# Kernel tuning notes

Measured on AMD Instinct MI355X. Metric: run time of the kernel, lower is better.

## Reference

```python
import jax, jax.numpy as jnp
import numpy as np

D_MODEL = 768
D_INNER = 1536      # expand*d_model
D_STATE = 128
NHEADS = 12         # d_inner // headdim
HEADDIM = 128
D_CONV = 4
CONV_DIM = D_INNER + 2 * D_STATE   # 1792 (ngroups=1)
D_IN_PROJ = 2 * D_INNER + 2 * D_STATE + NHEADS  # 3340


def setup_inputs() -> dict:
    key = jax.random.key(0)
    it = iter(jax.random.split(key, 24))
    def rn(shape, s):
        return jax.random.normal(next(it), shape, jnp.float32) * s
    inp = {}
    inp['x'] = jax.random.normal(next(it), (8, 12, 4096), jnp.float32)
    # conv stem
    inp['w1'] = rn((192, 12, 5), 0.2); inp['b1'] = jnp.zeros((192,))
    inp['bn1_g'] = jnp.ones((192,)); inp['bn1_b'] = jnp.zeros((192,)); inp['bn1_m'] = jnp.zeros((192,)); inp['bn1_v'] = jnp.ones((192,))
    inp['w2'] = rn((384, 192, 3), 0.05); inp['b2'] = jnp.zeros((384,))
    inp['bn2_g'] = jnp.ones((384,)); inp['bn2_b'] = jnp.zeros((384,)); inp['bn2_m'] = jnp.zeros((384,)); inp['bn2_v'] = jnp.ones((384,))
    inp['w3'] = rn((768, 384, 3), 0.05); inp['b3'] = jnp.zeros((768,))
    inp['bn3_g'] = jnp.ones((768,)); inp['bn3_b'] = jnp.zeros((768,)); inp['bn3_m'] = jnp.zeros((768,)); inp['bn3_v'] = jnp.ones((768,))
    # Mamba2 backbone
    inp['in_proj_w'] = rn((D_IN_PROJ, D_MODEL), 0.02)
    inp['conv_w'] = rn((CONV_DIM, D_CONV), 0.2)
    inp['conv_b'] = jnp.zeros((CONV_DIM,))
    inp['dt_bias'] = rn((NHEADS,), 0.5)
    inp['A_log'] = jnp.log(jax.random.uniform(next(it), (NHEADS,), minval=1.0, maxval=16.0))
    inp['D'] = jnp.ones((NHEADS,))
    inp['norm_w'] = jnp.ones((D_INNER,))
    inp['out_proj_w'] = rn((D_MODEL, D_INNER), 0.02)
    # classifier
    inp['fc1_w'] = rn((1024, 768), 0.02); inp['fc1_b'] = jnp.zeros((1024,))
    inp['bnc_g'] = jnp.ones((1024,)); inp['bnc_b'] = jnp.zeros((1024,)); inp['bnc_m'] = jnp.zeros((1024,)); inp['bnc_v'] = jnp.ones((1024,))
    inp['fc2_w'] = rn((27, 1024), 0.02); inp['fc2_b'] = jnp.zeros((27,))
    return inp


def _conv1d(x, w, b, stride, pad):
    y = jax.lax.conv_general_dilated(x, w, (stride,), [(pad, pad)], dimension_numbers=('NCH', 'OIH', 'NCH'))
    return y + b[None, :, None]


def _bn(x, g, b, m, v, eps=1e-5):
    sh = (1, -1, 1) if x.ndim == 3 else (1, -1)
    return (x - m.reshape(sh)) * jax.lax.rsqrt(v.reshape(sh) + eps) * g.reshape(sh) + b.reshape(sh)


def _forward(x, w1, b1, bn1_g, bn1_b, bn1_m, bn1_v, w2, b2, bn2_g, bn2_b, bn2_m, bn2_v,
             w3, b3, bn3_g, bn3_b, bn3_m, bn3_v, in_proj_w, conv_w, conv_b, dt_bias,
             A_log, D, norm_w, out_proj_w, fc1_w, fc1_b, bnc_g, bnc_b, bnc_m, bnc_v, fc2_w, fc2_b):
    gelu = lambda t: jax.nn.gelu(t, approximate=False)
    # conv stem (B, 12, 4096) -> (B, 768, 1024)
    h = _bn(gelu(_conv1d(x, w1, b1, 2, 2)), bn1_g, bn1_b, bn1_m, bn1_v)
    h = _bn(gelu(_conv1d(h, w2, b2, 2, 1)), bn2_g, bn2_b, bn2_m, bn2_v)
    h = _bn(gelu(_conv1d(h, w3, b3, 1, 1)), bn3_g, bn3_b, bn3_m, bn3_v)
    u = h.transpose(0, 2, 1)  # (B, L, 768)
    # Mamba2
    zxbcdt = u @ in_proj_w.T  # (B, L, 3340)
    z = zxbcdt[..., :D_INNER]
    xBC = zxbcdt[..., D_INNER:D_INNER + CONV_DIM]
    dt = jax.nn.softplus(zxbcdt[..., D_INNER + CONV_DIM:] + dt_bias)  # (B, L, H)
    # causal depthwise conv over time + silu
    xc = jax.lax.conv_general_dilated(xBC.transpose(0, 2, 1), conv_w[:, None, :], (1,), [(D_CONV - 1, 0)],
                                      dimension_numbers=('NCH', 'OIH', 'NCH'), feature_group_count=CONV_DIM)
    xBC = jax.nn.silu(xc + conv_b[None, :, None]).transpose(0, 2, 1)
    xs = xBC[..., :D_INNER]
    Bm = xBC[..., D_INNER:D_INNER + D_STATE]   # (B, L, N), ngroups=1
    Cm = xBC[..., D_INNER + D_STATE:]
    A = -jnp.exp(A_log)  # (H,)
    b_, l_ = xs.shape[0], xs.shape[1]
    xh = xs.reshape(b_, l_, NHEADS, HEADDIM)
    dA = jnp.exp(dt * A)  # (B, L, H)
    tm = lambda t: jnp.moveaxis(t, 1, 0)
    def step(state, inps):
        x_t, dA_t, dt_t, B_t, C_t = inps
        # state: (B, H, P, N)
        state = state * dA_t[..., None, None] + (dt_t[..., None] * x_t)[..., None] * B_t[:, None, None, :]
        y_t = jnp.einsum('bhpn,bn->bhp', state, C_t)
        return state, y_t
    state0 = jnp.zeros((b_, NHEADS, HEADDIM, D_STATE), xs.dtype)
    _, ys = jax.lax.scan(step, state0, (tm(xh), tm(dA), tm(dt), tm(Bm), tm(Cm)))
    y = jnp.moveaxis(ys, 0, 1) + D[None, None, :, None] * xh  # (B, L, H, P)
    y = y.reshape(b_, l_, D_INNER)
    # gated RMSNorm (norm_before_gate=False)
    y = y * jax.nn.silu(z)
    y = y * jax.lax.rsqrt(jnp.mean(y * y, axis=-1, keepdims=True) + 1e-5) * norm_w
    out = y @ out_proj_w.T  # (B, L, 768)
    rep = out.mean(axis=1)
    h1 = jax.nn.relu(_bn(rep @ fc1_w.T + fc1_b, bnc_g, bnc_b, bnc_m, bnc_v))
    return h1 @ fc2_w.T + fc2_b


def reference(x, w1, b1, bn1_g, bn1_b, bn1_m, bn1_v, w2, b2, bn2_g, bn2_b, bn2_m, bn2_v,
              w3, b3, bn3_g, bn3_b, bn3_m, bn3_v, in_proj_w, conv_w, conv_b, dt_bias,
              A_log, D, norm_w, out_proj_w, fc1_w, fc1_b, bnc_g, bnc_b, bnc_m, bnc_v, fc2_w, fc2_b):
    return _forward(x, w1, b1, bn1_g, bn1_b, bn1_m, bn1_v, w2, b2, bn2_g, bn2_b, bn2_m, bn2_v,
                    w3, b3, bn3_g, bn3_b, bn3_m, bn3_v, in_proj_w, conv_w, conv_b, dt_bias,
                    A_log, D, norm_w, out_proj_w, fc1_w, fc1_b, bnc_g, bnc_b, bnc_m, bnc_v, fc2_w, fc2_b)
```

## Files before the change

kernel.cpp:

```cpp
#include <hip/hip_runtime.h>
#include <math.h>

#define DEV __device__ __forceinline__

DEV float geluf(float x){ return 0.5f*x*(1.0f+erff(x*0.7071067811865476f)); }
DEV float siluf(float x){ return x/(1.0f+expf(-x)); }
DEV float softplusf(float x){ return fmaxf(x,0.0f)+log1pf(expf(-fabsf(x))); }
DEV unsigned short f2bf(float f){
  unsigned int u = __float_as_uint(f);
  unsigned int r = (u + 0x7fffu + ((u>>16)&1u)) >> 16;
  return (unsigned short)r;
}

typedef __attribute__((ext_vector_type(8))) short short8;
typedef __attribute__((ext_vector_type(4))) float f32x4;

__global__ void conv1_k(const float* __restrict__ x, const float* __restrict__ w,
                        const float* __restrict__ bias,
                        const float* __restrict__ g, const float* __restrict__ bb,
                        const float* __restrict__ m, const float* __restrict__ v,
                        float* __restrict__ out){
  int t  = blockIdx.x*256 + threadIdx.x;
  int og = blockIdx.y;
  int b  = blockIdx.z;
  const float* xb = x + (size_t)b*12*4096;
  float acc[8];
  #pragma unroll
  for(int oo=0;oo<8;++oo) acc[oo] = bias[og*8+oo];
  for(int i=0;i<12;++i){
    float xv[5];
    #pragma unroll
    for(int k=0;k<5;++k){
      int src = 2*t + k - 2;
      xv[k] = (src>=0 && src<4096) ? xb[i*4096+src] : 0.0f;
    }
    #pragma unroll
    for(int oo=0;oo<8;++oo){
      const float* wr = w + (size_t)(og*8+oo)*60 + i*5;
      #pragma unroll
      for(int k=0;k<5;++k) acc[oo] = fmaf(wr[k], xv[k], acc[oo]);
    }
  }
  #pragma unroll
  for(int oo=0;oo<8;++oo){
    int o = og*8+oo;
    float y = geluf(acc[oo]);
    float sc = g[o]*rsqrtf(v[o]+1e-5f);
    y = (y-m[o])*sc + bb[o];
    out[(size_t)b*192*2048 + (size_t)o*2048 + t] = y;
  }
}

__global__ void xpose1_k(const float* __restrict__ h1, unsigned short* __restrict__ T1){
  __shared__ float tile[32][33];
  int t0 = blockIdx.x*32, i0 = blockIdx.y*32, b = blockIdx.z;
  int c = threadIdx.x & 31, r4 = threadIdx.x >> 5;
  const float* src = h1 + (size_t)b*393216;
  #pragma unroll
  for(int i=0;i<4;++i){ int r = r4 + i*8; tile[r][c] = src[(size_t)(i0+r)*2048 + t0 + c]; }
  __syncthreads();
  unsigned short* dst = T1 + (size_t)b*2048*192;
  #pragma unroll
  for(int i=0;i<4;++i){ int r = r4 + i*8;
    dst[(size_t)(t0+r)*192 + i0 + c] = f2bf(tile[c][r]);
  }
}

__global__ void wr2_k(const float* __restrict__ w, unsigned short* __restrict__ wr){
  int gid = blockIdx.x*256 + threadIdx.x;
  if(gid < 221184){
    int o = gid / 576, rem = gid - o*576, k = rem / 192, i = rem - k*192;
    wr[gid] = f2bf(w[(size_t)o*576 + i*3 + k]);
  }
}
__global__ void wr3_k(const float* __restrict__ w, unsigned short* __restrict__ wr){
  int gid = blockIdx.x*256 + threadIdx.x;
  if(gid < 884736){
    int o = gid / 1152, rem = gid - o*1152, k = rem / 384, i = rem - k*384;
    wr[gid] = f2bf(w[(size_t)o*1152 + i*3 + k]);
  }
}

__global__ __launch_bounds__(256) void conv2_mfma(const unsigned short* __restrict__ A,
                                                  const unsigned short* __restrict__ W,
                                                  const float* __restrict__ bias,
                                                  const float* __restrict__ g, const float* __restrict__ bb,
                                                  const float* __restrict__ bm, const float* __restrict__ bv,
                                                  unsigned short* __restrict__ outb){
  __shared__ unsigned short As[4096], Bs[4096];
  const int tid = threadIdx.x;
  const int lane = tid & 63, wave = tid >> 6;
  const int wm = wave & 1, wn = wave >> 1;
  const int m0 = blockIdx.y*128, n0 = blockIdx.x*128;
  const int bidx = m0 >> 10, tloc = m0 & 1023;
  f32x4 acc[4][4];
  #pragma unroll
  for(int i=0;i<4;++i)
    #pragma unroll
    for(int j=0;j<4;++j) acc[i][j] = (f32x4){0.f,0.f,0.f,0.f};
  const int u0 = tid, u1 = tid + 256;
  const int r0 = u0>>2, kl0 = (u0&3) ^ ((r0>>1)&3);
  const int r1 = u1>>2, kl1 = (u1&3) ^ ((r1>>1)&3);
  const int kg = lane>>4, ml = lane&15;
  const short8 z8 = {0,0,0,0,0,0,0,0};
  for(int kb=0; kb<3; ++kb){
    int ta = 2*(tloc + r0) + kb - 1;
    int tb = 2*(tloc + r1) + kb - 1;
    bool va = (ta>=0) && (ta<2048);
    bool vb = (tb>=0) && (tb<2048);
    const unsigned short* pa = A + ((size_t)bidx*2048 + ta)*192;
    const unsigned short* pb = A + ((size_t)bidx*2048 + tb)*192;
    for(int c0=0; c0<192; c0+=32){
      int k0 = kb*192 + c0;
      short8 a0 = va ? *reinterpret_cast<const short8*>(pa + c0 + kl0*8) : z8;
      short8 a1 = vb ? *reinterpret_cast<const short8*>(pb + c0 + kl1*8) : z8;
      short8 b0 = *reinterpret_cast<const short8*>(W + (size_t)(n0+r0)*576 + k0 + kl0*8);
      short8 b1 = *reinterpret_cast<const short8*>(W + (size_t)(n0+r1)*576 + k0 + kl1*8);
      __syncthreads();
      *reinterpret_cast<short8*>(As + u0*8) = a0;
      *reinterpret_cast<short8*>(As + u1*8) = a1;
      *reinterpret_cast<short8*>(Bs + u0*8) = b0;
      *reinterpret_cast<short8*>(Bs + u1*8) = b1;
      __syncthreads();
      short8 af[4], bfr[4];
      #pragma unroll
      for(int f=0;f<4;++f){
        int row = wm*64 + f*16 + ml;
        int un  = row*4 + (kg ^ ((row>>1)&3));
        af[f] = *reinterpret_cast<const short8*>(As + un*8);
        int rowb = wn*64 + f*16 + ml;
        int ub   = rowb*4 + (kg ^ ((rowb>>1)&3));
        bfr[f] = *reinterpret_cast<const short8*>(Bs + ub*8);
      }
      #pragma unroll
      for(int i=0;i<4;++i)
        #pragma unroll
        for(int j=0;j<4;++j)
          acc[i][j] = __builtin_amdgcn_mfma_f32_16x16x32_bf16(af[i], bfr[j], acc[i][j], 0, 0, 0);
    }
  }
  #pragma unroll
  for(int i=0;i<4;++i){
    int rb = m0 + wm*64 + i*16 + kg*4;
    #pragma unroll
    for(int j=0;j<4;++j){
      int col = n0 + wn*64 + j*16 + ml;
      float sc = g[col]*rsqrtf(bv[col]+1e-5f);
      float mm = bm[col], bbv = bb[col], bi = bias[col];
      #pragma unroll
      for(int r=0;r<4;++r){
        float yv = geluf(acc[i][j][r] + bi);
        yv = (yv - mm)*sc + bbv;
        outb[(size_t)(rb+r)*384 + col] = f2bf(yv);
      }
    }
  }
}

__global__ __launch_bounds__(256) void conv3_mfma(const unsigned short* __restrict__ A,
                                                  const unsigned short* __restrict__ W,
                                                  const float* __restrict__ bias,
                                                  const float* __restrict__ g, const float* __restrict__ bb,
                                                  const float* __restrict__ bm, const float* __restrict__ bv,
                                                  unsigned short* __restrict__ outb,
                                                  float* __restrict__ outf){
  __shared__ unsigned short As[4096], Bs[4096];
  const int tid = threadIdx.x;
  const int lane = tid & 63, wave = tid >> 6;
  const int wm = wave & 1, wn = wave >> 1;
  const int m0 = blockIdx.y*128, n0 = blockIdx.x*128;
  const int bidx = m0 >> 10, tloc = m0 & 1023;
  f32x4 acc[4][4];
  #pragma unroll
  for(int i=0;i<4;++i)
    #pragma unroll
    for(int j=0;j<4;++j) acc[i][j] = (f32x4){0.f,0.f,0.f,0.f};
  const int u0 = tid, u1 = tid + 256;
  const int r0 = u0>>2, kl0 = (u0&3) ^ ((r0>>1)&3);
  const int r1 = u1>>2, kl1 = (u1&3) ^ ((r1>>1)&3);
  const int kg = lane>>4, ml = lane&15;
  const short8 z8 = {0,0,0,0,0,0,0,0};
  for(int kb=0; kb<3; ++kb){
    int ta = tloc + r0 + kb - 1;
    int tb = tloc + r1 + kb - 1;
    bool va = (ta>=0) && (ta<1024);
    bool vb = (tb>=0) && (tb<1024);
    const unsigned short* pa = A + ((size_t)bidx*1024 + ta)*384;
    const unsigned short* pb = A + ((size_t)bidx*1024 + tb)*384;
    for(int c0=0; c0<384; c0+=32){
      int k0 = kb*384 + c0;
      short8 a0 = va ? *reinterpret_cast<const short8*>(pa + c0 + kl0*8) : z8;
      short8 a1 = vb ? *reinterpret_cast<const short8*>(pb + c0 + kl1*8) : z8;
      short8 b0 = *reinterpret_cast<const short8*>(W + (size_t)(n0+r0)*1152 + k0 + kl0*8);
      short8 b1 = *reinterpret_cast<const short8*>(W + (size_t)(n0+r1)*1152 + k0 + kl1*8);
      __syncthreads();
      *reinterpret_cast<short8*>(As + u0*8) = a0;
      *reinterpret_cast<short8*>(As + u1*8) = a1;
      *reinterpret_cast<short8*>(Bs + u0*8) = b0;
      *reinterpret_cast<short8*>(Bs + u1*8) = b1;
      __syncthreads();
      short8 af[4], bfr[4];
      #pragma unroll
      for(int f=0;f<4;++f){
        int row = wm*64 + f*16 + ml;
        int un  = row*4 + (kg ^ ((row>>1)&3));
        af[f] = *reinterpret_cast<const short8*>(As + un*8);
        int rowb = wn*64 + f*16 + ml;
        int ub   = rowb*4 + (kg ^ ((rowb>>1)&3));
        bfr[f] = *reinterpret_cast<const short8*>(Bs + ub*8);
      }
      #pragma unroll
      for(int i=0;i<4;++i)
        #pragma unroll
        for(int j=0;j<4;++j)
          acc[i][j] = __builtin_amdgcn_mfma_f32_16x16x32_bf16(af[i], bfr[j], acc[i][j], 0, 0, 0);
    }
  }
  #pragma unroll
  for(int i=0;i<4;++i){
    int rb = m0 + wm*64 + i*16 + kg*4;
    #pragma unroll
    for(int j=0;j<4;++j){
      int col = n0 + wn*64 + j*16 + ml;
      float sc = g[col]*rsqrtf(bv[col]+1e-5f);
      float mm = bm[col], bbv = bb[col], bi = bias[col];
      #pragma unroll
      for(int r=0;r<4;++r){
        float yv = geluf(acc[i][j][r] + bi);
        yv = (yv - mm)*sc + bbv;
        outb[(size_t)(rb+r)*768 + col] = f2bf(yv);
        outf[(size_t)(rb+r)*768 + col] = yv;
      }
    }
  }
}

__global__ void wconv_k(const float* __restrict__ W, unsigned short* __restrict__ Wb){
  int i = (blockIdx.x*256 + threadIdx.x)*4;
  if(i < 2555904){
    float4 v = *reinterpret_cast<const float4*>(&W[i]);
    Wb[i+0] = f2bf(v.x); Wb[i+1] = f2bf(v.y); Wb[i+2] = f2bf(v.z); Wb[i+3] = f2bf(v.w);
  }
}

__global__ __launch_bounds__(256) void inproj_mfma(const unsigned short* __restrict__ A,
                                                   const unsigned short* __restrict__ B,
                                                   float* __restrict__ out){
  __shared__ unsigned short As[4096], Bs[4096];
  const int tid = threadIdx.x;
  const int lane = tid & 63, wave = tid >> 6;
  const int wm = wave & 1, wn = wave >> 1;
  const int m0 = blockIdx.y*128, n0 = blockIdx.x*128;
  f32x4 acc[4][4];
  #pragma unroll
  for(int i=0;i<4;++i)
    #pragma unroll
    for(int j=0;j<4;++j) acc[i][j] = (f32x4){0.f,0.f,0.f,0.f};
  const int u0 = tid, u1 = tid + 256;
  const int r0 = u0>>2, kl0 = (u0&3) ^ ((r0>>1)&3);
  const int r1 = u1>>2, kl1 = (u1&3) ^ ((r1>>1)&3);
  const int kg = lane>>4, ml = lane&15;
  for(int k0=0;k0<768;k0+=32){
    short8 a0 = *reinterpret_cast<const short8*>(A + (size_t)(m0+r0)*768 + k0 + kl0*8);
    short8 a1 = *reinterpret_cast<const short8*>(A + (size_t)(m0+r1)*768 + k0 + kl1*8);
    short8 b0 = *reinterpret_cast<const short8*>(B + (size_t)(n0+r0)*768 + k0 + kl0*8);
    short8 b1 = *reinterpret_cast<const short8*>(B + (size_t)(n0+r1)*768 + k0 + kl1*8);
    __syncthreads();
    *reinterpret_cast<short8*>(As + u0*8) = a0;
    *reinterpret_cast<short8*>(As + u1*8) = a1;
    *reinterpret_cast<short8*>(Bs + u0*8) = b0;
    *reinterpret_cast<short8*>(Bs + u1*8) = b1;
    __syncthreads();
    short8 af[4], bfr[4];
    #pragma unroll
    for(int f=0;f<4;++f){
      int row = wm*64 + f*16 + ml;
      int un  = row*4 + (kg ^ ((row>>1)&3));
      af[f] = *reinterpret_cast<const short8*>(As + un*8);
      int rowb = wn*64 + f*16 + ml;
      int ub   = rowb*4 + (kg ^ ((rowb>>1)&3));
      bfr[f] = *reinterpret_cast<const short8*>(Bs + ub*8);
    }
    #pragma unroll
    for(int i=0;i<4;++i)
      #pragma unroll
      for(int j=0;j<4;++j)
        acc[i][j] = __builtin_amdgcn_mfma_f32_16x16x32_bf16(af[i], bfr[j], acc[i][j], 0, 0, 0);
  }
  #pragma unroll
  for(int i=0;i<4;++i){
    int rb = m0 + wm*64 + i*16 + kg*4;
    #pragma unroll
    for(int j=0;j<4;++j){
      int col = n0 + wn*64 + j*16 + ml;
      #pragma unroll
      for(int r=0;r<4;++r)
        out[(size_t)(rb+r)*3340 + col] = acc[i][j][r];
    }
  }
}

__global__ __launch_bounds__(256) void dtgemm2_k(const float* __restrict__ h3f, const float* __restrict__ W,
                                                 const float* __restrict__ dt_bias, const float* __restrict__ A_log,
                                                 float* __restrict__ dt, float* __restrict__ dA){
  __shared__ float Ws[12][768];
  __shared__ float Ah[12], Bh[12];
  int tid = threadIdx.x;
  for(int idx=tid; idx<9216; idx+=256){
    int hh = idx/768, k = idx - hh*768;
    Ws[hh][k] = W[(size_t)(3328+hh)*768 + k];
  }
  if(tid<12){ Ah[tid] = -expf(A_log[tid]); Bh[tid] = dt_bias[tid]; }
  __syncthreads();
  int wave = tid>>6, lane = tid&63;
  int m = blockIdx.x*4 + wave;
  const float* xr = h3f + (size_t)m*768;
  float xv[12];
  #pragma unroll
  for(int q=0;q<12;++q) xv[q] = xr[q*64+lane];
  float res[12];
  #pragma unroll
  for(int h=0;h<12;++h){
    float acc = 0.f;
    #pragma unroll
    for(int q=0;q<12;++q) acc = fmaf(xv[q], Ws[h][q*64+lane], acc);
    #pragma unroll
    for(int off=32;off;off>>=1) acc += __shfl_xor(acc, off);
    res[h] = acc;
  }
  if(lane==0){
    #pragma unroll
    for(int h=0;h<12;++h){
      float sp = softplusf(res[h] + Bh[h]);
      dt[(size_t)m*12+h] = sp;
      dA[(size_t)m*12+h] = expf(sp*Ah[h]);
    }
  }
}

__global__ void dwconv_k(const float* __restrict__ zx, const float* __restrict__ cw,
                         const float* __restrict__ cb, float* __restrict__ xs,
                         float* __restrict__ Bo, float* __restrict__ Co){
  int gid = blockIdx.x*256 + threadIdx.x;
  int c = gid % 1792;
  int m = gid / 1792;
  int t = m & 1023;
  float4 w4 = *reinterpret_cast<const float4*>(&cw[c*4]);
  float wv[4] = {w4.x,w4.y,w4.z,w4.w};
  float acc = cb[c];
  #pragma unroll
  for(int j=0;j<4;++j){
    int tt = t - 3 + j;
    if(tt >= 0) acc = fmaf(wv[j], zx[(size_t)(m-3+j)*3340 + 1536 + c], acc);
  }
  float val = siluf(acc);
  if(c < 1536)       xs[(size_t)m*1536 + c]        = val;
  else if(c < 1664)  Bo[(size_t)m*128 + (c-1536)]  = val;
  else               Co[(size_t)m*128 + (c-1664)]  = val;
}

__global__ void cumda_k(const float* __restrict__ dA, float* __restrict__ cda){
  __shared__ float ld[1024];
  int bh = blockIdx.x; int b = bh/12, hh = bh - b*12;
  int tid = threadIdx.x;
  for(int i=tid;i<1024;i+=128) ld[i] = dA[((size_t)b*1024 + i)*12 + hh];
  __syncthreads();
  for(int c=0;c<8;++c){
    int base = c*128;
    for(int off=1;off<128;off<<=1){
      float v = ld[base+tid];
      if(tid>=off) v *= ld[base+tid-off];
      __syncthreads();
      ld[base+tid] = v;
      __syncthreads();
    }
  }
  for(int i=tid;i<1024;i+=128) cda[(size_t)bh*1024 + i] = ld[i];
}

#define SSTEP(E, BQE, CQE) \
  s[0][jj*4+E] = fmaf(s[0][jj*4+E], dav, c0*BQE); y0 = fmaf(s[0][jj*4+E], CQE, y0); \
  s[1][jj*4+E] = fmaf(s[1][jj*4+E], dav, c1*BQE); y1 = fmaf(s[1][jj*4+E], CQE, y1); \
  s[2][jj*4+E] = fmaf(s[2][jj*4+E], dav, c2*BQE); y2 = fmaf(s[2][jj*4+E], CQE, y2); \
  s[3][jj*4+E] = fmaf(s[3][jj*4+E], dav, c3*BQE); y3 = fmaf(s[3][jj*4+E], CQE, y3);

__global__ __launch_bounds__(128) void scan_chunk_k(float* __restrict__ xs,
    const float* __restrict__ Bm, const float* __restrict__ Cm,
    const float* __restrict__ dtb, const float* __restrict__ dAb,
    const float* __restrict__ Dv, float* __restrict__ sfin){
  const int c = blockIdx.x, h = blockIdx.y, b = blockIdx.z;
  const int tid = threadIdx.x;
  const int ng = tid & 3, pg = tid >> 2;
  __shared__ float lx[16][128], lB[16][144], lC[16][144], ly[16][128];
  __shared__ float ldt[16], lda_[16];
  float s[4][32];
  #pragma unroll
  for(int i=0;i<4;++i)
    #pragma unroll
    for(int j=0;j<32;++j) s[i][j]=0.f;
  const float Dh = Dv[h];
  const size_t mb = (size_t)b*1024 + (size_t)c*128;
  for(int t0=0;t0<128;t0+=16){
    for(int idx=tid; idx<2048; idx+=128){
      int tl = idx>>7, cc = idx&127;
      lx[tl][cc] = xs[(mb+t0+tl)*1536 + h*128 + cc];
      int slot = (cc>>5)*36 + (cc&31);
      lB[tl][slot] = Bm[(mb+t0+tl)*128 + cc];
      lC[tl][slot] = Cm[(mb+t0+tl)*128 + cc];
    }
    if(tid<16){
      ldt[tid]  = dtb[(mb+t0+tid)*12 + h];
      lda_[tid] = dAb[(mb+t0+tid)*12 + h];
    }
    __syncthreads();
    for(int tl=0; tl<16; ++tl){
      float dtv = ldt[tl], dav = lda_[tl];
      float4 xq = *reinterpret_cast<const float4*>(&lx[tl][pg*4]);
      float c0 = dtv*xq.x, c1 = dtv*xq.y, c2 = dtv*xq.z, c3 = dtv*xq.w;
      float y0=0.f,y1=0.f,y2=0.f,y3=0.f;
      #pragma unroll
      for(int jj=0;jj<8;++jj){
        float4 bq = *reinterpret_cast<const float4*>(&lB[tl][ng*36+jj*4]);
        float4 cq = *reinterpret_cast<const float4*>(&lC[tl][ng*36+jj*4]);
        SSTEP(0, bq.x, cq.x)
        SSTEP(1, bq.y, cq.y)
        SSTEP(2, bq.z, cq.z)
        SSTEP(3, bq.w, cq.w)
      }
      y0 += __shfl_xor(y0,1); y0 += __shfl_xor(y0,2);
      y1 += __shfl_xor(y1,1); y1 += __shfl_xor(y1,2);
      y2 += __shfl_xor(y2,1); y2 += __shfl_xor(y2,2);
      y3 += __shfl_xor(y3,1); y3 += __shfl_xor(y3,2);
      if(ng==0) *reinterpret_cast<float4*>(&ly[tl][pg*4]) = make_float4(y0,y1,y2,y3);
    }
    __syncthreads();
    for(int idx=tid; idx<2048; idx+=128){
      int tl = idx>>7, cc = idx&127;
      xs[(mb+t0+tl)*1536 + h*128 + cc] = ly[tl][cc] + Dh*lx[tl][cc];
    }
    __syncthreads();
  }
  float* dst = sfin + ((size_t)(b*12+h)*8 + c)*16384;
  #pragma unroll
  for(int jj=0;jj<8;++jj)
    #pragma unroll
    for(int e=0;e<4;++e){
      int n = ng*32 + jj*4 + e;
      *reinterpret_cast<float4*>(&dst[(size_t)n*128 + pg*4]) =
        make_float4(s[0][jj*4+e], s[1][jj*4+e], s[2][jj*4+e], s[3][jj*4+e]);
    }
}

__global__ __launch_bounds__(256) void correct_k(const float* __restrict__ Cm,
    const float* __restrict__ cumdA, const float* __restrict__ sfin,
    float* __restrict__ ys){
  const int c = blockIdx.x + 1, h = blockIdx.y, b = blockIdx.z;
  const int tid = threadIdx.x;
  const size_t bh = (size_t)b*12 + h;
  __shared__ float Sl[16][128];
  __shared__ float Cl[16][132];
  __shared__ float cumP[128];
  __shared__ float coefs[8];
  if(tid==0){
    float cf = 1.f;
    for(int cp=c-1; cp>=0; --cp){
      coefs[cp] = cf;
      cf *= cumdA[bh*1024 + (size_t)cp*128 + 127];
    }
  }
  if(tid<128) cumP[tid] = cumdA[bh*1024 + (size_t)c*128 + tid];
  __syncthreads();
  const int tp = tid>>4, tt = tid&15;
  float acc[8][8];
  #pragma unroll
  for(int i=0;i<8;++i)
    #pragma unroll
    for(int j=0;j<8;++j) acc[i][j]=0.f;
  const size_t mb = (size_t)b*1024 + (size_t)c*128;
  for(int n0=0;n0<128;n0+=16){
    {
      int kk = tid>>4, po = tid&15;
      float4 v0 = {0,0,0,0}, v1 = {0,0,0,0};
      for(int cp=0; cp<c; ++cp){
        const float* sp = sfin + ((bh*8 + cp)*16384) + (size_t)(n0+kk)*128 + po*8;
        float4 a0 = *reinterpret_cast<const float4*>(sp);
        float4 a1 = *reinterpret_cast<const float4*>(sp+4);
        float cf = coefs[cp];
        v0.x = fmaf(cf,a0.x,v0.x); v0.y = fmaf(cf,a0.y,v0.y);
        v0.z = fmaf(cf,a0.z,v0.z); v0.w = fmaf(cf,a0.w,v0.w);
        v1.x = fmaf(cf,a1.x,v1.x); v1.y = fmaf(cf,a1.y,v1.y);
        v1.z = fmaf(cf,a1.z,v1.z); v1.w = fmaf(cf,a1.w,v1.w);
      }
      *reinterpret_cast<float4*>(&Sl[kk][po*8])   = v0;
      *reinterpret_cast<float4*>(&Sl[kk][po*8+4]) = v1;
    }
    #pragma unroll
    for(int e=0;e<8;++e){
      int idx = tid*8 + e; int tl = idx>>4, kk = idx&15;
      Cl[kk][tl] = Cm[(mb + tl)*128 + n0 + kk];
    }
    __syncthreads();
    #pragma unroll
    for(int kk=0;kk<16;++kk){
      float4 sa = *reinterpret_cast<const float4*>(&Sl[kk][tp*8]);
      float4 sb = *reinterpret_cast<const float4*>(&Sl[kk][tp*8+4]);
      float4 ca = *reinterpret_cast<const float4*>(&Cl[kk][tt*8]);
      float4 cb = *reinterpret_cast<const float4*>(&Cl[kk][tt*8+4]);
      float sv[8] = {sa.x,sa.y,sa.z,sa.w,sb.x,sb.y,sb.z,sb.w};
      float cv[8] = {ca.x,ca.y,ca.z,ca.w,cb.x,cb.y,cb.z,cb.w};
      #pragma unroll
      for(int i=0;i<8;++i)
        #pragma unroll
        for(int j=0;j<8;++j) acc[i][j] = fmaf(sv[i], cv[j], acc[i][j]);
    }
    __syncthreads();
  }
  #pragma unroll
  for(int j=0;j<8;++j){
    int tl = tt*8 + j;
    float cp = cumP[tl];
    float* yp = ys + (mb + tl)*1536 + h*128 + tp*8;
    float4 y0 = *reinterpret_cast<float4*>(yp);
    float4 y1 = *reinterpret_cast<float4*>(yp+4);
    y0.x += cp*acc[0][j]; y0.y += cp*acc[1][j]; y0.z += cp*acc[2][j]; y0.w += cp*acc[3][j];
    y1.x += cp*acc[4][j]; y1.y += cp*acc[5][j]; y1.z += cp*acc[6][j]; y1.w += cp*acc[7][j];
    *reinterpret_cast<float4*>(yp)   = y0;
    *reinterpret_cast<float4*>(yp+4) = y1;
  }
}

__global__ void gate_k(const float* __restrict__ ys, const float* __restrict__ zx,
                       const float* __restrict__ nw, float* __restrict__ ybp){
  int m = blockIdx.x;
  int b = m >> 10, t = m & 1023;
  int tid = threadIdx.x;
  float gvals[6];
  float ss = 0.0f;
  #pragma unroll
  for(int r=0;r<6;++r){
    int c = r*256 + tid;
    float yv = ys[(size_t)m*1536 + c];
    float zv = zx[(size_t)m*3340 + c];
    float gv = yv * siluf(zv);
    gvals[r] = gv;
    ss = fmaf(gv, gv, ss);
  }
  #pragma unroll
  for(int off=32;off;off>>=1) ss += __shfl_xor(ss, off);
  __shared__ float red[4];
  if((tid&63)==0) red[tid>>6] = ss;
  __syncthreads();
  float tot = red[0]+red[1]+red[2]+red[3];
  float scale = rsqrtf(tot*(1.0f/1536.0f) + 1e-5f);
  float* dst = ybp + ((size_t)(t&7)*8 + b)*1536;
  #pragma unroll
  for(int r=0;r<6;++r){
    int c = r*256 + tid;
    atomicAdd(&dst[c], gvals[r]*scale*nw[c]);
  }
}

__global__ void ybm_k(const float* __restrict__ ybp, float* __restrict__ ybm){
  int idx = blockIdx.x*256 + threadIdx.x;
  float s = 0.0f;
  #pragma unroll
  for(int p=0;p<8;++p) s += ybp[(size_t)p*12288 + idx];
  ybm[idx] = s * (1.0f/1024.0f);
}

__global__ void rep_k(const float* __restrict__ ybm, const float* __restrict__ W,
                      float* __restrict__ rep){
  int wid  = (blockIdx.x<<2) + (threadIdx.x>>6);
  int lane = threadIdx.x & 63;
  int b = wid / 768, o = wid % 768;
  const float* xr = ybm + (size_t)b*1536;
  const float* wr = W + (size_t)o*1536;
  float acc = 0.0f;
  for(int c=lane;c<1536;c+=64) acc = fmaf(xr[c], wr[c], acc);
  #pragma unroll
  for(int off=32;off;off>>=1) acc += __shfl_xor(acc, off);
  if(lane==0) rep[wid] = acc;
}

__global__ void fc1_k(const float* __restrict__ rep, const float* __restrict__ W,
                      const float* __restrict__ bias, const float* __restrict__ g,
                      const float* __restrict__ bb, const float* __restrict__ m,
                      const float* __restrict__ v, float* __restrict__ out){
  int wid  = (blockIdx.x<<2) + (threadIdx.x>>6);
  int lane = threadIdx.x & 63;
  int b = wid >> 10, o = wid & 1023;
  const float* xr = rep + (size_t)b*768;
  const float* wr = W + (size_t)o*768;
  float acc = 0.0f;
  for(int c=lane;c<768;c+=64) acc = fmaf(xr[c], wr[c], acc);
  #pragma unroll
  for(int off=32;off;off>>=1) acc += __shfl_xor(acc, off);
  if(lane==0){
    float val = acc + bias[o];
    float sc = g[o]*rsqrtf(v[o]+1e-5f);
    val = (val - m[o])*sc + bb[o];
    out[wid] = fmaxf(val, 0.0f);
  }
}

__global__ void fc2_k(const float* __restrict__ h1, const float* __restrict__ W,
                      const float* __restrict__ bias, float* __restrict__ out){
  int wid  = (blockIdx.x<<2) + (threadIdx.x>>6);
  int lane = threadIdx.x & 63;
  int b = wid / 27, o = wid % 27;
  const float* xr = h1 + (size_t)b*1024;
  const float* wr = W + (size_t)o*1024;
  float acc = 0.0f;
  for(int c=lane;c<1024;c+=64) acc = fmaf(xr[c], wr[c], acc);
  #pragma unroll
  for(int off=32;off;off>>=1) acc += __shfl_xor(acc, off);
  if(lane==0) out[wid] = acc + bias[o];
}

#define OFF_H1     0u
#define OFF_T1     3145728u
#define OFF_T2     4718592u
#define OFF_H3T    6291456u
#define OFF_WB     9437184u
#define OFF_W2R    10715136u
#define OFF_W3R    10825728u
#define OFF_ZX     12582912u
#define OFF_XS     39944192u
#define OFF_H3F    39944192u
#define OFF_B      52527104u
#define OFF_C      53575680u
#define OFF_DT     54624256u
#define OFF_DA     54722560u
#define OFF_SLOT98K 54820864u
#define OFF_YBM    54919168u
#define OFF_REP    54931456u
#define OFF_FC1    54937600u
#define OFF_SFIN   0u

extern "C" void kernel_launch(void* const* d_in, const int* in_sizes, int n_in,
                              void* d_out, int out_size, void* d_ws, size_t ws_size,
                              hipStream_t stream){
  const float* x       = (const float*)d_in[0];
  const float* w1      = (const float*)d_in[1];
  const float* b1      = (const float*)d_in[2];
  const float* bn1g    = (const float*)d_in[3];
  const float* bn1b    = (const float*)d_in[4];
  const float* bn1m    = (const float*)d_in[5];
  const float* bn1v    = (const float*)d_in[6];
  const float* w2      = (const float*)d_in[7];
  const float* b2      = (const float*)d_in[8];
  const float* bn2g    = (const float*)d_in[9];
  const float* bn2b    = (const float*)d_in[10];
  const float* bn2m    = (const float*)d_in[11];
  const float* bn2v    = (const float*)d_in[12];
  const float* w3      = (const float*)d_in[13];
  const float* b3      = (const float*)d_in[14];
  const float* bn3g    = (const float*)d_in[15];
  const float* bn3b    = (const float*)d_in[16];
  const float* bn3m    = (const float*)d_in[17];
  const float* bn3v    = (const float*)d_in[18];
  const float* ipw     = (const float*)d_in[19];
  const float* convw   = (const float*)d_in[20];
  const float* convb   = (const float*)d_in[21];
  const float* dtbias  = (const float*)d_in[22];
  const float* Alog    = (const float*)d_in[23];
  const float* Dvec    = (const float*)d_in[24];
  const float* normw   = (const float*)d_in[25];
  const float* opw     = (const float*)d_in[26];
  const float* fc1w    = (const float*)d_in[27];
  const float* fc1b    = (const float*)d_in[28];
  const float* bncg    = (const float*)d_in[29];
  const float* bncb    = (const float*)d_in[30];
  const float* bncm    = (const float*)d_in[31];
  const float* bncv    = (const float*)d_in[32];
  const float* fc2w    = (const float*)d_in[33];
  const float* fc2b    = (const float*)d_in[34];

  float* ws   = (float*)d_ws;
  float* h1   = ws + OFF_H1;
  unsigned short* T1  = (unsigned short*)(ws + OFF_T1);
  unsigned short* T2  = (unsigned short*)(ws + OFF_T2);
  unsigned short* h3t = (unsigned short*)(ws + OFF_H3T);
  unsigned short* Wb  = (unsigned short*)(ws + OFF_WB);
  unsigned short* w2r = (unsigned short*)(ws + OFF_W2R);
  unsigned short* w3r = (unsigned short*)(ws + OFF_W3R);
  float* zx   = ws + OFF_ZX;
  float* xsb  = ws + OFF_XS;
  float* h3f  = ws + OFF_H3F;
  float* Bb   = ws + OFF_B;
  float* Cb   = ws + OFF_C;
  float* dtb  = ws + OFF_DT;
  float* dAb  = ws + OFF_DA;
  float* slot = ws + OFF_SLOT98K;
  float* ybm  = ws + OFF_YBM;
  float* rep  = ws + OFF_REP;
  float* f1b  = ws + OFF_FC1;
  float* sfin = ws + OFF_SFIN;
  float* outp = (float*)d_out;

  conv1_k<<<dim3(8,24,8),  256, 0, stream>>>(x, w1, b1, bn1g, bn1b, bn1m, bn1v, h1);
  xpose1_k<<<dim3(64,6,8), 256, 0, stream>>>(h1, T1);
  wconv_k<<<2496, 256, 0, stream>>>(ipw, Wb);
  wr2_k<<<864, 256, 0, stream>>>(w2, w2r);
  wr3_k<<<3456, 256, 0, stream>>>(w3, w3r);
  conv2_mfma<<<dim3(3,64), 256, 0, stream>>>(T1, w2r, b2, bn2g, bn2b, bn2m, bn2v, T2);
  conv3_mfma<<<dim3(6,64), 256, 0, stream>>>(T2, w3r, b3, bn3g, bn3b, bn3m, bn3v, h3t, h3f);
  dtgemm2_k<<<2048, 256, 0, stream>>>(h3f, ipw, dtbias, Alog, dtb, dAb);
  inproj_mfma<<<dim3(26,64), 256, 0, stream>>>(h3t, Wb, zx);
  dwconv_k<<<57344, 256, 0, stream>>>(zx, convw, convb, xsb, Bb, Cb);
  cumda_k<<<96, 128, 0, stream>>>(dAb, slot);
  scan_chunk_k<<<dim3(8,12,8), 128, 0, stream>>>(xsb, Bb, Cb, dtb, dAb, Dvec, sfin);
  correct_k<<<dim3(7,12,8), 256, 0, stream>>>(Cb, slot, sfin, xsb);
  hipMemsetAsync(slot, 0, 98304*sizeof(float), stream);
  gate_k<<<8192, 256, 0, stream>>>(xsb, zx, normw, slot);
  ybm_k<<<48, 256, 0, stream>>>(slot, ybm);
  rep_k<<<1536, 256, 0, stream>>>(ybm, opw, rep);
  fc1_k<<<2048, 256, 0, stream>>>(rep, fc1w, fc1b, bncg, bncb, bncm, bncv, f1b);
  fc2_k<<<54, 256, 0, stream>>>(f1b, fc2w, fc2b, outp);
}
```

Measured before the change: 743.8 us.

## Split in_proj output, vectorize dwconv, widen scan tile, replace atomics with reduction

Several independent changes land together. The three weight-prep kernels are merged into one launch, and inproj now stages tiles through global_load_lds and writes z and xBC into separate compact buffers. dwconv is vectorized to four channels per thread over the contiguous xBC buffer, and the chunked scan gives each thread 8 P-values by 16 N-states instead of 4 by 32. The gate kernel drops the atomicAdd time-mean in favour of storing the gated output and reducing it with a two-stage deterministic sum. These aim to cut launch overhead, strided and uncoalesced traffic, and atomic contention, at the cost of an extra full-size write and read of the gated activations and higher scan register pressure.

```diff
diff --git a/kernel.cpp b/kernel.cpp
--- a/kernel.cpp
+++ b/kernel.cpp
@@ -14,6 +14,12 @@
 
 typedef __attribute__((ext_vector_type(8))) short short8;
 typedef __attribute__((ext_vector_type(4))) float f32x4;
+
+typedef const __attribute__((address_space(1))) unsigned int GU;
+typedef __attribute__((address_space(3))) unsigned int LU;
+DEV void gload16(const void* g, void* l){
+  __builtin_amdgcn_global_load_lds((GU*)g, (LU*)l, 16, 0, 0);
+}
 
 __global__ void conv1_k(const float* __restrict__ x, const float* __restrict__ w,
                         const float* __restrict__ bias,
@@ -66,18 +72,20 @@
   }
 }
 
-__global__ void wr2_k(const float* __restrict__ w, unsigned short* __restrict__ wr){
+__global__ void wprep_k(const float* __restrict__ ipw, const float* __restrict__ w2,
+                        const float* __restrict__ w3, unsigned short* __restrict__ Wb,
+                        unsigned short* __restrict__ w2r, unsigned short* __restrict__ w3r){
   int gid = blockIdx.x*256 + threadIdx.x;
-  if(gid < 221184){
-    int o = gid / 576, rem = gid - o*576, k = rem / 192, i = rem - k*192;
-    wr[gid] = f2bf(w[(size_t)o*576 + i*3 + k]);
-  }
-}
-__global__ void wr3_k(const float* __restrict__ w, unsigned short* __restrict__ wr){
-  int gid = blockIdx.x*256 + threadIdx.x;
-  if(gid < 884736){
-    int o = gid / 1152, rem = gid - o*1152, k = rem / 384, i = rem - k*384;
-    wr[gid] = f2bf(w[(size_t)o*1152 + i*3 + k]);
+  if(gid < 2555904){
+    Wb[gid] = f2bf(ipw[gid]);
+  } else if(gid < 2555904+221184){
+    int g2 = gid - 2555904;
+    int o = g2 / 576, rem = g2 - o*576, k = rem / 192, i = rem - k*192;
+    w2r[g2] = f2bf(w2[(size_t)o*576 + i*3 + k]);
+  } else if(gid < 2555904+221184+884736){
+    int g3 = gid - 2555904 - 221184;
+    int o = g3 / 1152, rem = g3 - o*1152, k = rem / 384, i = rem - k*384;
+    w3r[g3] = f2bf(w3[(size_t)o*1152 + i*3 + k]);
   }
 }
 
@@ -235,17 +243,9 @@
   }
 }
 
-__global__ void wconv_k(const float* __restrict__ W, unsigned short* __restrict__ Wb){
-  int i = (blockIdx.x*256 + threadIdx.x)*4;
-  if(i < 2555904){
-    float4 v = *reinterpret_cast<const float4*>(&W[i]);
-    Wb[i+0] = f2bf(v.x); Wb[i+1] = f2bf(v.y); Wb[i+2] = f2bf(v.z); Wb[i+3] = f2bf(v.w);
-  }
-}
-
 __global__ __launch_bounds__(256) void inproj_mfma(const unsigned short* __restrict__ A,
                                                    const unsigned short* __restrict__ B,
-                                                   float* __restrict__ out){
+                                                   float* __restrict__ Z, float* __restrict__ XB){
   __shared__ unsigned short As[4096], Bs[4096];
   const int tid = threadIdx.x;
   const int lane = tid & 63, wave = tid >> 6;
@@ -256,20 +256,20 @@
   for(int i=0;i<4;++i)
     #pragma unroll
     for(int j=0;j<4;++j) acc[i][j] = (f32x4){0.f,0.f,0.f,0.f};
-  const int u0 = tid, u1 = tid + 256;
-  const int r0 = u0>>2, kl0 = (u0&3) ^ ((r0>>1)&3);
-  const int r1 = u1>>2, kl1 = (u1&3) ^ ((r1>>1)&3);
+  const int u1 = tid + 256;
+  const int r0 = tid>>2, kl0 = (tid&3) ^ ((r0>>1)&3);
+  const int r1 = u1>>2,  kl1 = (u1&3) ^ ((r1>>1)&3);
   const int kg = lane>>4, ml = lane&15;
+  unsigned short* a0d = As + wave*512;
+  unsigned short* a1d = As + 2048 + wave*512;
+  unsigned short* b0d = Bs + wave*512;
+  unsigned short* b1d = Bs + 2048 + wave*512;
   for(int k0=0;k0<768;k0+=32){
-    short8 a0 = *reinterpret_cast<const short8*>(A + (size_t)(m0+r0)*768 + k0 + kl0*8);
-    short8 a1 = *reinterpret_cast<const short8*>(A + (size_t)(m0+r1)*768 + k0 + kl1*8);
-    short8 b0 = *reinterpret_cast<const short8*>(B + (size_t)(n0+r0)*768 + k0 + kl0*8);
-    short8 b1 = *reinterpret_cast<const short8*>(B + (size_t)(n0+r1)*768 + k0 + kl1*8);
     __syncthreads();
-    *reinterpret_cast<short8*>(As + u0*8) = a0;
-    *reinterpret_cast<short8*>(As + u1*8) = a1;
-    *reinterpret_cast<short8*>(Bs + u0*8) = b0;
-    *reinterpret_cast<short8*>(Bs + u1*8) = b1;
+    gload16(A + (size_t)(m0+r0)*768 + k0 + kl0*8, a0d);
+    gload16(A + (size_t)(m0+r1)*768 + k0 + kl1*8, a1d);
+    gload16(B + (size_t)(n0+r0)*768 + k0 + kl0*8, b0d);
+    gload16(B + (size_t)(n0+r1)*768 + k0 + kl1*8, b1d);
     __syncthreads();
     short8 af[4], bfr[4];
     #pragma unroll
@@ -287,15 +287,18 @@
       for(int j=0;j<4;++j)
         acc[i][j] = __builtin_amdgcn_mfma_f32_16x16x32_bf16(af[i], bfr[j], acc[i][j], 0, 0, 0);
   }
+  float* op; int cb; int stride;
+  if(n0 < 1536){ op = Z;  cb = n0;        stride = 1536; }
+  else         { op = XB; cb = n0 - 1536; stride = 1792; }
   #pragma unroll
   for(int i=0;i<4;++i){
     int rb = m0 + wm*64 + i*16 + kg*4;
     #pragma unroll
     for(int j=0;j<4;++j){
-      int col = n0 + wn*64 + j*16 + ml;
+      int col = cb + wn*64 + j*16 + ml;
       #pragma unroll
       for(int r=0;r<4;++r)
-        out[(size_t)(rb+r)*3340 + col] = acc[i][j][r];
+        op[(size_t)(rb+r)*stride + col] = acc[i][j][r];
     }
   }
 }
@@ -338,25 +341,35 @@
   }
 }
 
-__global__ void dwconv_k(const float* __restrict__ zx, const float* __restrict__ cw,
+__global__ void dwconv_k(const float* __restrict__ XB, const float* __restrict__ cw,
                          const float* __restrict__ cb, float* __restrict__ xs,
                          float* __restrict__ Bo, float* __restrict__ Co){
   int gid = blockIdx.x*256 + threadIdx.x;
-  int c = gid % 1792;
-  int m = gid / 1792;
+  int c4 = gid % 448;
+  int m = gid / 448;
   int t = m & 1023;
-  float4 w4 = *reinterpret_cast<const float4*>(&cw[c*4]);
-  float wv[4] = {w4.x,w4.y,w4.z,w4.w};
-  float acc = cb[c];
+  int c = c4*4;
+  float wA[4][4];
+  #pragma unroll
+  for(int i=0;i<4;++i)
+    *reinterpret_cast<float4*>(wA[i]) = *reinterpret_cast<const float4*>(&cw[(c+i)*4]);
+  float4 bi = *reinterpret_cast<const float4*>(&cb[c]);
+  float av[4] = {bi.x, bi.y, bi.z, bi.w};
   #pragma unroll
   for(int j=0;j<4;++j){
     int tt = t - 3 + j;
-    if(tt >= 0) acc = fmaf(wv[j], zx[(size_t)(m-3+j)*3340 + 1536 + c], acc);
-  }
-  float val = siluf(acc);
-  if(c < 1536)       xs[(size_t)m*1536 + c]        = val;
-  else if(c < 1664)  Bo[(size_t)m*128 + (c-1536)]  = val;
-  else               Co[(size_t)m*128 + (c-1664)]  = val;
+    if(tt >= 0){
+      float4 xv = *reinterpret_cast<const float4*>(&XB[(size_t)(m-3+j)*1792 + c]);
+      av[0] = fmaf(wA[0][j], xv.x, av[0]);
+      av[1] = fmaf(wA[1][j], xv.y, av[1]);
+      av[2] = fmaf(wA[2][j], xv.z, av[2]);
+      av[3] = fmaf(wA[3][j], xv.w, av[3]);
+    }
+  }
+  float4 res = make_float4(siluf(av[0]), siluf(av[1]), siluf(av[2]), siluf(av[3]));
+  if(c4 < 384)      *reinterpret_cast<float4*>(&xs[(size_t)m*1536 + c])        = res;
+  else if(c4 < 416) *reinterpret_cast<float4*>(&Bo[(size_t)m*128 + (c-1536)])  = res;
+  else              *reinterpret_cast<float4*>(&Co[(size_t)m*128 + (c-1664)])  = res;
 }
 
 __global__ void cumda_k(const float* __restrict__ dA, float* __restrict__ cda){
@@ -378,35 +391,29 @@
   for(int i=tid;i<1024;i+=128) cda[(size_t)bh*1024 + i] = ld[i];
 }
 
-#define SSTEP(E, BQE, CQE) \
-  s[0][jj*4+E] = fmaf(s[0][jj*4+E], dav, c0*BQE); y0 = fmaf(s[0][jj*4+E], CQE, y0); \
-  s[1][jj*4+E] = fmaf(s[1][jj*4+E], dav, c1*BQE); y1 = fmaf(s[1][jj*4+E], CQE, y1); \
-  s[2][jj*4+E] = fmaf(s[2][jj*4+E], dav, c2*BQE); y2 = fmaf(s[2][jj*4+E], CQE, y2); \
-  s[3][jj*4+E] = fmaf(s[3][jj*4+E], dav, c3*BQE); y3 = fmaf(s[3][jj*4+E], CQE, y3);
-
 __global__ __launch_bounds__(128) void scan_chunk_k(float* __restrict__ xs,
     const float* __restrict__ Bm, const float* __restrict__ Cm,
     const float* __restrict__ dtb, const float* __restrict__ dAb,
     const float* __restrict__ Dv, float* __restrict__ sfin){
   const int c = blockIdx.x, h = blockIdx.y, b = blockIdx.z;
   const int tid = threadIdx.x;
-  const int ng = tid & 3, pg = tid >> 2;
-  __shared__ float lx[16][128], lB[16][144], lC[16][144], ly[16][128];
+  const int ng = tid & 7, pg = tid >> 3;
+  __shared__ float lx[16][128], lB[16][160], lC[16][160], ly[16][128];
   __shared__ float ldt[16], lda_[16];
-  float s[4][32];
-  #pragma unroll
-  for(int i=0;i<4;++i)
-    #pragma unroll
-    for(int j=0;j<32;++j) s[i][j]=0.f;
+  float s[8][16];
+  #pragma unroll
+  for(int i=0;i<8;++i)
+    #pragma unroll
+    for(int j=0;j<16;++j) s[i][j]=0.f;
   const float Dh = Dv[h];
   const size_t mb = (size_t)b*1024 + (size_t)c*128;
   for(int t0=0;t0<128;t0+=16){
     for(int idx=tid; idx<2048; idx+=128){
       int tl = idx>>7, cc = idx&127;
       lx[tl][cc] = xs[(mb+t0+tl)*1536 + h*128 + cc];
-      int slot = (cc>>5)*36 + (cc&31);
-      lB[tl][slot] = Bm[(mb+t0+tl)*128 + cc];
-      lC[tl][slot] = Cm[(mb+t0+tl)*128 + cc];
+      int sl = (cc>>4)*20 + (cc&15);
+      lB[tl][sl] = Bm[(mb+t0+tl)*128 + cc];
+      lC[tl][sl] = Cm[(mb+t0+tl)*128 + cc];
     }
     if(tid<16){
       ldt[tid]  = dtb[(mb+t0+tid)*12 + h];
@@ -415,23 +422,34 @@
     __syncthreads();
     for(int tl=0; tl<16; ++tl){
       float dtv = ldt[tl], dav = lda_[tl];
-      float4 xq = *reinterpret_cast<const float4*>(&lx[tl][pg*4]);
-      float c0 = dtv*xq.x, c1 = dtv*xq.y, c2 = dtv*xq.z, c3 = dtv*xq.w;
-      float y0=0.f,y1=0.f,y2=0.f,y3=0.f;
-      #pragma unroll
-      for(int jj=0;jj<8;++jj){
-        float4 bq = *reinterpret_cast<const float4*>(&lB[tl][ng*36+jj*4]);
-        float4 cq = *reinterpret_cast<const float4*>(&lC[tl][ng*36+jj*4]);
-        SSTEP(0, bq.x, cq.x)
-        SSTEP(1, bq.y, cq.y)
-        SSTEP(2, bq.z, cq.z)
-        SSTEP(3, bq.w, cq.w)
+      float4 xa = *reinterpret_cast<const float4*>(&lx[tl][pg*8]);
+      float4 xb_ = *reinterpret_cast<const float4*>(&lx[tl][pg*8+4]);
+      float cc_[8] = {dtv*xa.x, dtv*xa.y, dtv*xa.z, dtv*xa.w,
+                      dtv*xb_.x, dtv*xb_.y, dtv*xb_.z, dtv*xb_.w};
+      float y[8] = {0.f,0.f,0.f,0.f,0.f,0.f,0.f,0.f};
+      #pragma unroll
+      for(int jj=0;jj<4;++jj){
+        float4 bq = *reinterpret_cast<const float4*>(&lB[tl][ng*20+jj*4]);
+        float4 cq = *reinterpret_cast<const float4*>(&lC[tl][ng*20+jj*4]);
+        float bv[4]={bq.x,bq.y,bq.z,bq.w}, cv[4]={cq.x,cq.y,cq.z,cq.w};
+        #pragma unroll
+        for(int p=0;p<8;++p)
+          #pragma unroll
+          for(int e=0;e<4;++e){
+            s[p][jj*4+e] = fmaf(s[p][jj*4+e], dav, cc_[p]*bv[e]);
+            y[p] = fmaf(s[p][jj*4+e], cv[e], y[p]);
+          }
       }
-      y0 += __shfl_xor(y0,1); y0 += __shfl_xor(y0,2);
-      y1 += __shfl_xor(y1,1); y1 += __shfl_xor(y1,2);
-      y2 += __shfl_xor(y2,1); y2 += __shfl_xor(y2,2);
-      y3 += __shfl_xor(y3,1); y3 += __shfl_xor(y3,2);
-      if(ng==0) *reinterpret_cast<float4*>(&ly[tl][pg*4]) = make_float4(y0,y1,y2,y3);
+      #pragma unroll
+      for(int p=0;p<8;++p){
+        y[p] += __shfl_xor(y[p],1);
+        y[p] += __shfl_xor(y[p],2);
+        y[p] += __shfl_xor(y[p],4);
+      }
+      if(ng==0){
+        *reinterpret_cast<float4*>(&ly[tl][pg*8])   = make_float4(y[0],y[1],y[2],y[3]);
+        *reinterpret_cast<float4*>(&ly[tl][pg*8+4]) = make_float4(y[4],y[5],y[6],y[7]);
+      }
     }
     __syncthreads();
     for(int idx=tid; idx<2048; idx+=128){
@@ -442,12 +460,14 @@
   }
   float* dst = sfin + ((size_t)(b*12+h)*8 + c)*16384;
   #pragma unroll
-  for(int jj=0;jj<8;++jj)
+  for(int jj=0;jj<4;++jj)
     #pragma unroll
     for(int e=0;e<4;++e){
-      int n = ng*32 + jj*4 + e;
-      *reinterpret_cast<float4*>(&dst[(size_t)n*128 + pg*4]) =
+      int n = ng*16 + jj*4 + e;
+      *reinterpret_cast<float4*>(&dst[(size_t)n*128 + pg*8]) =
         make_float4(s[0][jj*4+e], s[1][jj*4+e], s[2][jj*4+e], s[3][jj*4+e]);
+      *reinterpret_cast<float4*>(&dst[(size_t)n*128 + pg*8+4]) =
+        make_float4(s[4][jj*4+e], s[5][jj*4+e], s[6][jj*4+e], s[7][jj*4+e]);
     }
 }
 
@@ -529,10 +549,9 @@
   }
 }
 
-__global__ void gate_k(const float* __restrict__ ys, const float* __restrict__ zx,
-                       const float* __restrict__ nw, float* __restrict__ ybp){
+__global__ void gate_k(const float* __restrict__ ys, const float* __restrict__ Z,
+                       const float* __restrict__ nw, float* __restrict__ ysc){
   int m = blockIdx.x;
-  int b = m >> 10, t = m & 1023;
   int tid = threadIdx.x;
   float gvals[6];
   float ss = 0.0f;
@@ -540,7 +559,7 @@
   for(int r=0;r<6;++r){
     int c = r*256 + tid;
     float yv = ys[(size_t)m*1536 + c];
-    float zv = zx[(size_t)m*3340 + c];
+    float zv = Z[(size_t)m*1536 + c];
     float gv = yv * siluf(zv);
     gvals[r] = gv;
     ss = fmaf(gv, gv, ss);
@@ -552,19 +571,31 @@
   __syncthreads();
   float tot = red[0]+red[1]+red[2]+red[3];
   float scale = rsqrtf(tot*(1.0f/1536.0f) + 1e-5f);
-  float* dst = ybp + ((size_t)(t&7)*8 + b)*1536;
   #pragma unroll
   for(int r=0;r<6;++r){
     int c = r*256 + tid;
-    atomicAdd(&dst[c], gvals[r]*scale*nw[c]);
-  }
-}
-
-__global__ void ybm_k(const float* __restrict__ ybp, float* __restrict__ ybm){
+    ysc[(size_t)m*1536 + c] = gvals[r]*scale*nw[c];
+  }
+}
+
+__global__ void ysum_k(const float* __restrict__ ysc, float* __restrict__ part){
+  int bid = blockIdx.x;
+  int bb = bid / 48, rem = bid % 48;
+  int cs = rem / 8, tc = rem % 8;
+  int col = cs*256 + threadIdx.x;
+  const float* base = ysc + ((size_t)bb*1024 + tc*128)*1536 + col;
+  float s = 0.f;
+  for(int r=0;r<128;++r) s += base[(size_t)r*1536];
+  part[((size_t)(bb*6+cs)*8 + tc)*256 + threadIdx.x] = s;
+}
+
+__global__ void ybm2_k(const float* __restrict__ part, float* __restrict__ ybm){
   int idx = blockIdx.x*256 + threadIdx.x;
-  float s = 0.0f;
-  #pragma unroll
-  for(int p=0;p<8;++p) s += ybp[(size_t)p*12288 + idx];
+  int bb = idx / 1536, cc = idx % 1536;
+  int cs = cc / 256, ci = cc % 256;
+  float s = 0.f;
+  #pragma unroll
+  for(int tc=0;tc<8;++tc) s += part[((size_t)(bb*6+cs)*8 + tc)*256 + ci];
   ybm[idx] = s * (1.0f/1024.0f);
 }
 
@@ -624,7 +655,8 @@
 #define OFF_WB     9437184u
 #define OFF_W2R    10715136u
 #define OFF_W3R    10825728u
-#define OFF_ZX     12582912u
+#define OFF_Z      12582912u
+#define OFF_XB     25165824u
 #define OFF_XS     39944192u
 #define OFF_H3F    39944192u
 #define OFF_B      52527104u
@@ -684,7 +716,8 @@
   unsigned short* Wb  = (unsigned short*)(ws + OFF_WB);
   unsigned short* w2r = (unsigned short*)(ws + OFF_W2R);
   unsigned short* w3r = (unsigned short*)(ws + OFF_W3R);
-  float* zx   = ws + OFF_ZX;
+  float* Zb   = ws + OFF_Z;
+  float* XBb  = ws + OFF_XB;
   float* xsb  = ws + OFF_XS;
   float* h3f  = ws + OFF_H3F;
   float* Bb   = ws + OFF_B;
@@ -696,24 +729,23 @@
   float* rep  = ws + OFF_REP;
   float* f1b  = ws + OFF_FC1;
   float* sfin = ws + OFF_SFIN;
+  float* ysc  = ws + OFF_SFIN;
   float* outp = (float*)d_out;
 
   conv1_k<<<dim3(8,24,8),  256, 0, stream>>>(x, w1, b1, bn1g, bn1b, bn1m, bn1v, h1);
   xpose1_k<<<dim3(64,6,8), 256, 0, stream>>>(h1, T1);
-  wconv_k<<<2496, 256, 0, stream>>>(ipw, Wb);
-  wr2_k<<<864, 256, 0, stream>>>(w2, w2r);
-  wr3_k<<<3456, 256, 0, stream>>>(w3, w3r);
+  wprep_k<<<14304, 256, 0, stream>>>(ipw, w2, w3, Wb, w2r, w3r);
   conv2_mfma<<<dim3(3,64), 256, 0, stream>>>(T1, w2r, b2, bn2g, bn2b, bn2m, bn2v, T2);
   conv3_mfma<<<dim3(6,64), 256, 0, stream>>>(T2, w3r, b3, bn3g, bn3b, bn3m, bn3v, h3t, h3f);
   dtgemm2_k<<<2048, 256, 0, stream>>>(h3f, ipw, dtbias, Alog, dtb, dAb);
-  inproj_mfma<<<dim3(26,64), 256, 0, stream>>>(h3t, Wb, zx);
-  dwconv_k<<<57344, 256, 0, stream>>>(zx, convw, convb, xsb, Bb, Cb);
+  inproj_mfma<<<dim3(26,64), 256, 0, stream>>>(h3t, Wb, Zb, XBb);
+  dwconv_k<<<14336, 256, 0, stream>>>(XBb, convw, convb, xsb, Bb, Cb);
   cumda_k<<<96, 128, 0, stream>>>(dAb, slot);
   scan_chunk_k<<<dim3(8,12,8), 128, 0, stream>>>(xsb, Bb, Cb, dtb, dAb, Dvec, sfin);
   correct_k<<<dim3(7,12,8), 256, 0, stream>>>(Cb, slot, sfin, xsb);
-  hipMemsetAsync(slot, 0, 98304*sizeof(float), stream);
-  gate_k<<<8192, 256, 0, stream>>>(xsb, zx, normw, slot);
-  ybm_k<<<48, 256, 0, stream>>>(slot, ybm);
+  gate_k<<<8192, 256, 0, stream>>>(xsb, Zb, normw, ysc);
+  ysum_k<<<384, 256, 0, stream>>>(ysc, slot);
+  ybm2_k<<<48, 256, 0, stream>>>(slot, ybm);
   rep_k<<<1536, 256, 0, stream>>>(ybm, opw, rep);
   fc1_k<<<2048, 256, 0, stream>>>(rep, fc1w, fc1b, bncg, bncb, bncm, bncv, f1b);
   fc2_k<<<54, 256, 0, stream>>>(f1b, fc2w, fc2b, outp);
```

Result: slower. 845.1 us (+13.6%).
